# Optimization experiments

Hardware: AMD Instinct MI355X
Metric: run time of the kernel (lower is better)

The kernel has to match this reference:

```python
import jax, jax.numpy as jnp
import numpy as np

B, S, D_IN, D_HID, D_OUT = 32, 512, 768, 3072, 768


def setup_inputs() -> dict:
    key = jax.random.key(0)
    k1, k2, k3, k4 = jax.random.split(key, 4)
    init_k = float(np.sqrt(1.0 / D_IN))
    init_k2 = float(np.sqrt(1.0 / D_HID))
    x = jax.random.normal(k1, (B, S, D_IN), dtype=jnp.float32)
    in_weight = jax.random.uniform(k2, (D_HID, D_IN), dtype=jnp.float32, minval=-init_k, maxval=init_k)
    in_bias = jax.random.uniform(k3, (D_HID,), dtype=jnp.float32, minval=-init_k, maxval=init_k)
    out_weight = jax.random.uniform(k4, (D_HID, D_OUT), dtype=jnp.float32, minval=-init_k2, maxval=init_k2)
    return {"x": x, "in_weight": in_weight, "in_bias": in_bias, "out_weight": out_weight}


def reference(x, in_weight, in_bias, out_weight):
    # flatten leading dims to tokens: [B*S, D_IN]
    lead = x.shape[:-1]
    xt = x.reshape(-1, in_weight.shape[1])
    # hidden = GELU(x @ W_in^T + b)   (in_weight stored [hidden, in])
    h = jax.nn.gelu(jnp.einsum('td,hd->th', xt, in_weight) + in_bias, approximate=False)
    # out = hidden @ W_out            (out_weight stored [hidden, out]; no output bias)
    out = jnp.einsum('th,ho->to', h, out_weight)
    return out.reshape(*lead, out_weight.shape[1])
```

## Files before the change

kernel.cpp:

```cpp
#include <hip/hip_runtime.h>

typedef short bf16x8 __attribute__((ext_vector_type(8)));
typedef float f32x4  __attribute__((ext_vector_type(4)));

__device__ __forceinline__ unsigned short f2bf(float f) {
    unsigned int u = __float_as_uint(f);
    u += 0x7FFFu + ((u >> 16) & 1u);
    return (unsigned short)(u >> 16);
}

__device__ __forceinline__ float gelu_f(float x) {
    float x2 = x * x;
    float u = x * (-1.5957691216f - 0.0713548162f * x2);
    float e = __expf(u);
    return x * __builtin_amdgcn_rcpf(1.0f + e);
}

__global__ void cvt_f32_bf16(const float* __restrict__ in,
                             unsigned short* __restrict__ out, int n4) {
    int stride = gridDim.x * blockDim.x;
    for (int i = blockIdx.x * blockDim.x + threadIdx.x; i < n4; i += stride) {
        float4 v = ((const float4*)in)[i];
        ushort4 r;
        r.x = f2bf(v.x); r.y = f2bf(v.y); r.z = f2bf(v.z); r.w = f2bf(v.w);
        ((ushort4*)out)[i] = r;
    }
}

__global__ void transpose_cvt(const float* __restrict__ in,
                              unsigned short* __restrict__ out, int H, int O) {
    __shared__ float tile[32][33];
    int o0 = blockIdx.x * 32, h0 = blockIdx.y * 32;
    int tx = threadIdx.x, ty = threadIdx.y;
    #pragma unroll
    for (int r = 0; r < 32; r += 8)
        tile[ty + r][tx] = in[(size_t)(h0 + ty + r) * O + o0 + tx];
    __syncthreads();
    #pragma unroll
    for (int r = 0; r < 32; r += 8) {
        int o = ty + r;
        out[(size_t)(o0 + o) * H + h0 + tx] = f2bf(tile[tx][o]);
    }
}

template <int EPI, int K, int N>
__global__ __launch_bounds__(512, 4) void gemm_bt(
    const unsigned short* __restrict__ A,
    const unsigned short* __restrict__ B,
    const float* __restrict__ bias,
    void* __restrict__ Cp) {
    constexpr int BHALF = 16384;
    constexpr int LBUF  = 24576;
    __shared__ __align__(16) char lds[2 * LBUF];
    const int t = threadIdx.x;
    const int w = t >> 6, l = t & 63;
    constexpr int ntiles = N >> 7;

    int bid = blockIdx.x;
    int nwg = gridDim.x;
    int wgid = ((nwg & 7) == 0) ? ((bid & 7) * (nwg >> 3) + (bid >> 3)) : bid;
    const int mt = wgid / ntiles, nt = wgid % ntiles;
    const int m0 = mt << 8, n0 = nt << 7;
    const int wr = w >> 1, wc = w & 1;

    auto stage = [&](int kt, char* dst) {
        const int kb = kt << 5;
        #pragma unroll
        for (int p = 0; p < 2; ++p) {
            int idx = p * 512 + t;
            int prow = idx >> 3;
            int lg = (idx & 7) ^ (prow & 7);
            const unsigned short* ga =
                A + (size_t)(m0 + (lg >> 2) * 128 + prow) * K + kb + (lg & 3) * 8;
            __builtin_amdgcn_global_load_lds(
                (const __attribute__((address_space(1))) void*)ga,
                (__attribute__((address_space(3))) void*)(dst + idx * 16), 16, 0, 0);
        }
        {
            int prow = t >> 3;
            int lg = (t & 7) ^ (prow & 7);
            const unsigned short* gb =
                B + (size_t)(n0 + (lg >> 2) * 64 + prow) * K + kb + (lg & 3) * 8;
            __builtin_amdgcn_global_load_lds(
                (const __attribute__((address_space(1))) void*)gb,
                (__attribute__((address_space(3))) void*)(dst + BHALF + t * 16), 16, 0, 0);
        }
    };

    const int ks = l >> 4, lr = l & 15;
    int aoff[4], boff[4];
    #pragma unroll
    for (int mi = 0; mi < 4; ++mi) {
        int prow = (wr & 1) * 64 + mi * 16 + lr;
        int lg   = ((wr >> 1) << 2) + ks;
        aoff[mi] = prow * 128 + ((lg ^ (prow & 7)) << 4);
    }
    #pragma unroll
    for (int ni = 0; ni < 4; ++ni) {
        int prow = ni * 16 + lr;
        int lg   = (wc << 2) + ks;
        boff[ni] = BHALF + prow * 128 + ((lg ^ (prow & 7)) << 4);
    }

    f32x4 acc[4][4];
    {
        f32x4 z = {0.f, 0.f, 0.f, 0.f};
        #pragma unroll
        for (int i = 0; i < 4; ++i)
            #pragma unroll
            for (int j = 0; j < 4; ++j) acc[i][j] = z;
    }

    constexpr int NT = K >> 5;
    stage(0, lds);
    __builtin_amdgcn_sched_barrier(0);
    asm volatile("" ::: "memory");
    stage(1, lds + LBUF);

    for (int kt = 0; kt < NT; ++kt) {
        asm volatile("s_waitcnt vmcnt(3)\n\ts_barrier" ::: "memory");
        __builtin_amdgcn_sched_barrier(0);
        const char* base = lds + (kt & 1) * LBUF;
        bf16x8 bv[4], av[2];
        #pragma unroll
        for (int ni = 0; ni < 4; ++ni) bv[ni] = *(const bf16x8*)(base + boff[ni]);
        av[0] = *(const bf16x8*)(base + aoff[0]);
        av[1] = *(const bf16x8*)(base + aoff[1]);
        #pragma unroll
        for (int mi = 0; mi < 2; ++mi)
            #pragma unroll
            for (int ni = 0; ni < 4; ++ni)
                acc[mi][ni] = __builtin_amdgcn_mfma_f32_16x16x32_bf16(
                    av[mi], bv[ni], acc[mi][ni], 0, 0, 0);
        av[0] = *(const bf16x8*)(base + aoff[2]);
        av[1] = *(const bf16x8*)(base + aoff[3]);
        #pragma unroll
        for (int mi = 0; mi < 2; ++mi)
            #pragma unroll
            for (int ni = 0; ni < 4; ++ni)
                acc[2 + mi][ni] = __builtin_amdgcn_mfma_f32_16x16x32_bf16(
                    av[mi], bv[ni], acc[2 + mi][ni], 0, 0, 0);
        __builtin_amdgcn_sched_barrier(0);
        asm volatile("s_waitcnt lgkmcnt(0)\n\ts_barrier" ::: "memory");
        __builtin_amdgcn_sched_barrier(0);
        stage(kt + 2 < NT ? kt + 2 : NT - 1, lds + (kt & 1) * LBUF);
    }

    const int colb = n0 + wc * 64 + lr;
    if constexpr (EPI == 0) {
        unsigned short* Cb = (unsigned short*)Cp;
        float bvs[4];
        #pragma unroll
        for (int ni = 0; ni < 4; ++ni) bvs[ni] = bias[colb + ni * 16];
        #pragma unroll
        for (int mi = 0; mi < 4; ++mi)
            #pragma unroll
            for (int j = 0; j < 4; ++j) {
                size_t row = m0 + wr * 64 + mi * 16 + ((l >> 4) << 2) + j;
                #pragma unroll
                for (int ni = 0; ni < 4; ++ni) {
                    float v = acc[mi][ni][j] + bvs[ni];
                    Cb[row * N + colb + ni * 16] = f2bf(gelu_f(v));
                }
            }
    } else {
        float* Cf = (float*)Cp;
        #pragma unroll
        for (int mi = 0; mi < 4; ++mi)
            #pragma unroll
            for (int j = 0; j < 4; ++j) {
                size_t row = m0 + wr * 64 + mi * 16 + ((l >> 4) << 2) + j;
                #pragma unroll
                for (int ni = 0; ni < 4; ++ni)
                    Cf[row * N + colb + ni * 16] = acc[mi][ni][j];
            }
    }
}

extern "C" void kernel_launch(void* const* d_in, const int* in_sizes, int n_in,
                              void* d_out, int out_size, void* d_ws, size_t ws_size,
                              hipStream_t stream) {
    const float* x  = (const float*)d_in[0];
    const float* w1 = (const float*)d_in[1];
    const float* b1 = (const float*)d_in[2];
    const float* w2 = (const float*)d_in[3];
    float* out = (float*)d_out;

    const int T = 16384, DIN = 768, DH = 3072, DOUT = 768;

    unsigned short* xb  = (unsigned short*)d_ws;
    unsigned short* w1b = xb  + (size_t)T * DIN;
    unsigned short* w2t = w1b + (size_t)DH * DIN;
    unsigned short* h   = w2t + (size_t)DOUT * DH;

    size_t fixed = ((size_t)T * DIN + (size_t)DH * DIN + (size_t)DOUT * DH) * 2;
    int CH = T;
    while (CH > 256 && fixed + (size_t)CH * DH * 2 > ws_size) CH >>= 1;

    cvt_f32_bf16<<<2048, 256, 0, stream>>>(x, xb, T * DIN / 4);
    cvt_f32_bf16<<<1024, 256, 0, stream>>>(w1, w1b, DH * DIN / 4);
    transpose_cvt<<<dim3(DOUT / 32, DH / 32), dim3(32, 8), 0, stream>>>(w2, w2t, DH, DOUT);

    for (int c0 = 0; c0 < T; c0 += CH) {
        gemm_bt<0, 768, 3072><<<(CH / 256) * (DH / 128), 512, 0, stream>>>(
            xb + (size_t)c0 * DIN, w1b, b1, h);
        gemm_bt<1, 3072, 768><<<(CH / 256) * (DOUT / 128), 512, 0, stream>>>(
            h, w2t, b1, out + (size_t)c0 * DOUT);
    }
}
```

Baseline: 207.6 us.

## Triple-buffer first GEMM and add 256x192 BK64 tile kernel for second GEMM

The first GEMM moves from double to triple buffering in LDS, prefetching three K-tiles ahead with an adjusted vmcnt wait. The second GEMM (K=3072, N=768) gets a new kernel with a 256x192 output tile and a K step of 64. Each wave computes 128x48 with an 8x3 accumulator array, which cuts the number of K iterations and barriers and raises MFMA work per LDS load. The trade-off is more LDS and registers per block, so fewer blocks fit per CU (launch bound 2). With 192-wide tiles the grid becomes 256 blocks.

Measured after the change: 196.7 us. 5.2% less time.

```diff
diff --git a/kernel.cpp b/kernel.cpp
--- a/kernel.cpp
+++ b/kernel.cpp
@@ -44,14 +44,14 @@
 }
 
 template <int EPI, int K, int N>
-__global__ __launch_bounds__(512, 4) void gemm_bt(
+__global__ __launch_bounds__(512, 4) void gemm_k1(
     const unsigned short* __restrict__ A,
     const unsigned short* __restrict__ B,
     const float* __restrict__ bias,
     void* __restrict__ Cp) {
     constexpr int BHALF = 16384;
     constexpr int LBUF  = 24576;
-    __shared__ __align__(16) char lds[2 * LBUF];
+    __shared__ __align__(16) char lds[3 * LBUF];
     const int t = threadIdx.x;
     const int w = t >> 6, l = t & 63;
     constexpr int ntiles = N >> 7;
@@ -116,11 +116,14 @@
     __builtin_amdgcn_sched_barrier(0);
     asm volatile("" ::: "memory");
     stage(1, lds + LBUF);
+    __builtin_amdgcn_sched_barrier(0);
+    asm volatile("" ::: "memory");
+    stage(2, lds + 2 * LBUF);
 
     for (int kt = 0; kt < NT; ++kt) {
-        asm volatile("s_waitcnt vmcnt(3)\n\ts_barrier" ::: "memory");
-        __builtin_amdgcn_sched_barrier(0);
-        const char* base = lds + (kt & 1) * LBUF;
+        asm volatile("s_waitcnt vmcnt(6)\n\ts_barrier" ::: "memory");
+        __builtin_amdgcn_sched_barrier(0);
+        const char* base = lds + (kt % 3) * LBUF;
         bf16x8 bv[4], av[2];
         #pragma unroll
         for (int ni = 0; ni < 4; ++ni) bv[ni] = *(const bf16x8*)(base + boff[ni]);
@@ -143,7 +146,7 @@
         __builtin_amdgcn_sched_barrier(0);
         asm volatile("s_waitcnt lgkmcnt(0)\n\ts_barrier" ::: "memory");
         __builtin_amdgcn_sched_barrier(0);
-        stage(kt + 2 < NT ? kt + 2 : NT - 1, lds + (kt & 1) * LBUF);
+        stage(kt + 3 < NT ? kt + 3 : NT - 1, lds + (kt % 3) * LBUF);
     }
 
     const int colb = n0 + wc * 64 + lr;
@@ -174,6 +177,143 @@
                 for (int ni = 0; ni < 4; ++ni)
                     Cf[row * N + colb + ni * 16] = acc[mi][ni][j];
             }
+    }
+}
+
+template <int EPI, int K, int N>
+__global__ __launch_bounds__(512, 2) void gemm_k2(
+    const unsigned short* __restrict__ A,
+    const unsigned short* __restrict__ B,
+    const float* __restrict__ bias,
+    void* __restrict__ Cp) {
+    constexpr int BN = 192, NREP = 3;
+    constexpr int BHALF = 32768;
+    constexpr int LBUF  = BHALF + BN * 128;
+    __shared__ __align__(16) char lds[2 * LBUF];
+    const int t = threadIdx.x;
+    const int w = t >> 6, l = t & 63;
+    constexpr int ntiles = N / BN;
+
+    int bid = blockIdx.x;
+    int nwg = gridDim.x;
+    int wgid = ((nwg & 7) == 0) ? ((bid & 7) * (nwg >> 3) + (bid >> 3)) : bid;
+    const int mt = wgid / ntiles, nt = wgid % ntiles;
+    const int m0 = mt << 8, n0 = nt * BN;
+    const int wr = w >> 2, wc = w & 3;
+
+    const int rA = t >> 3;
+    const int sl = (t & 7) ^ (rA & 7);
+
+    auto stage = [&](int kt, char* dst) {
+        const int kc = kt * 64 + sl * 8;
+        #pragma unroll
+        for (int i = 0; i < 4; ++i) {
+            const unsigned short* ga = A + (size_t)(m0 + i * 64 + rA) * K + kc;
+            char* la = dst + i * 8192 + (w << 10);
+            __builtin_amdgcn_global_load_lds((const __attribute__((address_space(1))) void*)ga,
+                                             (__attribute__((address_space(3))) void*)la, 16, 0, 0);
+        }
+        #pragma unroll
+        for (int i = 0; i < NREP; ++i) {
+            const unsigned short* gb = B + (size_t)(n0 + i * 64 + rA) * K + kc;
+            char* lb = dst + BHALF + i * 8192 + (w << 10);
+            __builtin_amdgcn_global_load_lds((const __attribute__((address_space(1))) void*)gb,
+                                             (__attribute__((address_space(3))) void*)lb, 16, 0, 0);
+        }
+    };
+
+    const int swz = ((l >> 4) ^ (l & 7)) << 4;
+    const int aoff0 = (wr * 128 + (l & 15)) * 128 + swz;
+    const int aoffX = aoff0 ^ 64;
+    const int boff0 = BHALF + (wc * (BN / 4) + (l & 15)) * 128 + swz;
+    const int boffX = boff0 ^ 64;
+
+    f32x4 acc[8][NREP];
+    {
+        f32x4 z = {0.f, 0.f, 0.f, 0.f};
+        #pragma unroll
+        for (int i = 0; i < 8; ++i)
+            #pragma unroll
+            for (int j = 0; j < NREP; ++j) acc[i][j] = z;
+    }
+
+    constexpr int NT = K >> 6;
+    stage(0, lds);
+    __builtin_amdgcn_sched_barrier(0);
+    asm volatile("" ::: "memory");
+    stage(1, lds + LBUF);
+
+    for (int kt = 0; kt < NT; ++kt) {
+        asm volatile("s_waitcnt vmcnt(7)\n\ts_barrier" ::: "memory");
+        __builtin_amdgcn_sched_barrier(0);
+        const char* base = lds + (kt & 1) * LBUF;
+        bf16x8 av[4][2], bv[NREP][2];
+        #pragma unroll
+        for (int ni = 0; ni < NREP; ++ni) {
+            bv[ni][0] = *(const bf16x8*)(base + boff0 + ni * 2048);
+            bv[ni][1] = *(const bf16x8*)(base + boffX + ni * 2048);
+        }
+        #pragma unroll
+        for (int mi = 0; mi < 4; ++mi) {
+            av[mi][0] = *(const bf16x8*)(base + aoff0 + mi * 2048);
+            av[mi][1] = *(const bf16x8*)(base + aoffX + mi * 2048);
+        }
+        #pragma unroll
+        for (int ksel = 0; ksel < 2; ++ksel)
+            #pragma unroll
+            for (int mi = 0; mi < 4; ++mi)
+                #pragma unroll
+                for (int ni = 0; ni < NREP; ++ni)
+                    acc[mi][ni] = __builtin_amdgcn_mfma_f32_16x16x32_bf16(
+                        av[mi][ksel], bv[ni][ksel], acc[mi][ni], 0, 0, 0);
+        #pragma unroll
+        for (int mi = 0; mi < 4; ++mi) {
+            av[mi][0] = *(const bf16x8*)(base + aoff0 + (4 + mi) * 2048);
+            av[mi][1] = *(const bf16x8*)(base + aoffX + (4 + mi) * 2048);
+        }
+        #pragma unroll
+        for (int ksel = 0; ksel < 2; ++ksel)
+            #pragma unroll
+            for (int mi = 0; mi < 4; ++mi)
+                #pragma unroll
+                for (int ni = 0; ni < NREP; ++ni)
+                    acc[4 + mi][ni] = __builtin_amdgcn_mfma_f32_16x16x32_bf16(
+                        av[mi][ksel], bv[ni][ksel], acc[4 + mi][ni], 0, 0, 0);
+        __builtin_amdgcn_sched_barrier(0);
+        asm volatile("s_waitcnt lgkmcnt(0)\n\ts_barrier" ::: "memory");
+        __builtin_amdgcn_sched_barrier(0);
+        stage(kt + 2 < NT ? kt + 2 : NT - 1, lds + (kt & 1) * LBUF);
+    }
+
+    if constexpr (EPI == 0) {
+        unsigned short* Cb = (unsigned short*)Cp;
+        #pragma unroll
+        for (int ni = 0; ni < NREP; ++ni) {
+            int col = n0 + wc * (BN / 4) + ni * 16 + (l & 15);
+            float bvs = bias[col];
+            #pragma unroll
+            for (int mi = 0; mi < 8; ++mi) {
+                int rbase = m0 + wr * 128 + mi * 16 + ((l >> 4) << 2);
+                #pragma unroll
+                for (int j = 0; j < 4; ++j) {
+                    float v = acc[mi][ni][j] + bvs;
+                    Cb[(size_t)(rbase + j) * N + col] = f2bf(gelu_f(v));
+                }
+            }
+        }
+    } else {
+        float* Cf = (float*)Cp;
+        #pragma unroll
+        for (int ni = 0; ni < NREP; ++ni) {
+            int col = n0 + wc * (BN / 4) + ni * 16 + (l & 15);
+            #pragma unroll
+            for (int mi = 0; mi < 8; ++mi) {
+                int rbase = m0 + wr * 128 + mi * 16 + ((l >> 4) << 2);
+                #pragma unroll
+                for (int j = 0; j < 4; ++j)
+                    Cf[(size_t)(rbase + j) * N + col] = acc[mi][ni][j];
+            }
+        }
     }
 }
 
@@ -202,9 +342,9 @@
     transpose_cvt<<<dim3(DOUT / 32, DH / 32), dim3(32, 8), 0, stream>>>(w2, w2t, DH, DOUT);
 
     for (int c0 = 0; c0 < T; c0 += CH) {
-        gemm_bt<0, 768, 3072><<<(CH / 256) * (DH / 128), 512, 0, stream>>>(
+        gemm_k1<0, 768, 3072><<<(CH / 256) * (DH / 128), 512, 0, stream>>>(
             xb + (size_t)c0 * DIN, w1b, b1, h);
-        gemm_bt<1, 3072, 768><<<(CH / 256) * (DOUT / 128), 512, 0, stream>>>(
+        gemm_k2<1, 3072, 768><<<(CH / 256) * (DOUT / 192), 512, 0, stream>>>(
             h, w2t, b1, out + (size_t)c0 * DOUT);
     }
 }
```
